# Optimization experiments

Hardware: AMD Instinct MI355X
Metric: run time of the kernel (lower is better)

## Reference

```python
import jax, jax.numpy as jnp
import numpy as np
import math

NH, KS, KR, VS, HID, RS = 8, 32, 8, 32, 256, 16
TOTAL = 2 * KS + VS + KR  # 104


def setup_inputs() -> dict:
    key = jax.random.key(0)
    ks = jax.random.split(key, 10)
    B, S = 4, 512
    H = jax.random.normal(ks[0], (B, S, HID), dtype=jnp.float32)
    route_data = jax.random.normal(ks[1], (B, S, S, RS), dtype=jnp.float32)
    attention_mask = jnp.zeros((B, 1, 1, S), dtype=jnp.float32)
    W_qkv = jax.random.normal(ks[2], (NH * TOTAL, HID), dtype=jnp.float32) * 0.02
    Wd = jax.random.normal(ks[3], (NH * KR, RS), dtype=jnp.float32) * 0.02
    Wroute = jax.random.normal(ks[4], (NH * VS, RS), dtype=jnp.float32) * 0.02
    W_out = jax.random.normal(ks[5], (HID, NH * VS), dtype=jnp.float32) * 0.02
    b_out = jnp.zeros((HID,), dtype=jnp.float32)
    ln_w = jnp.ones((HID,), dtype=jnp.float32)
    ln_b = jnp.zeros((HID,), dtype=jnp.float32)
    return {"H": H, "route_data": route_data, "attention_mask": attention_mask,
            "W_qkv": W_qkv, "Wd": Wd, "Wroute": Wroute,
            "W_out": W_out, "b_out": b_out, "ln_w": ln_w, "ln_b": ln_b}


def reference(H, route_data, attention_mask, W_qkv, Wd, Wroute, W_out, b_out, ln_w, ln_b):
    B, S, _ = H.shape
    # fused QKVQr projection: [B,S,NH,TOTAL] -> [B,NH,S,TOTAL]
    H2 = (H @ W_qkv.T).reshape(B, S, NH, TOTAL).transpose(0, 2, 1, 3)
    Qn = H2[..., :KS]
    Kn = H2[..., KS:2 * KS]
    V = H2[..., 2 * KS:2 * KS + VS]
    Qr = H2[..., 2 * KS + VS:]
    # route keys: [B,i,j,NH,KR]
    Kr = (route_data @ Wd.T).reshape(B, S, S, NH, KR)
    QKr = jnp.einsum('bhik,bijhk->bhij', Qr, Kr)
    scale = 1.0 / math.sqrt(KS + KR)
    scores = scale * (jnp.einsum('bhik,bhjk->bhij', Qn, Kn) + QKr) + attention_mask
    probs = jax.nn.softmax(scores, axis=-1)
    ctx = jnp.einsum('bhij,bhjv->bhiv', probs, V)
    # route values: [B,i,j,NH,VS]
    Vr = (route_data @ Wroute.T).reshape(B, S, S, NH, VS)
    ctx = ctx + jnp.einsum('bhij,bijhv->bhiv', probs, Vr)
    ctx = ctx.transpose(0, 2, 1, 3).reshape(B, S, NH * VS)
    # output projection + TF-style LayerNorm, residual added AFTER norm
    out = ctx @ W_out.T + b_out
    u = out.mean(-1, keepdims=True)
    s = ((out - u) ** 2).mean(-1, keepdims=True)
    ln = ln_w * (out - u) / jnp.sqrt(s + 1e-12) + ln_b
    return ln + H
```

## Files before the change

kernel.cpp:

```cpp
#include <hip/hip_runtime.h>
#include <cmath>

#define B_    4
#define S_    512
#define NH_   8
#define TOT_  104
#define NQKV_ 832
#define ROWS_ 2048

typedef float f32x4 __attribute__((ext_vector_type(4)));
typedef short short8 __attribute__((ext_vector_type(8)));

__device__ inline float bfu2f(unsigned int bits16) {
  union { unsigned int i; float f; } v; v.i = bits16 << 16; return v.f;
}
__device__ inline unsigned short f2bf(float f) {
  union { float f; unsigned int i; } v; v.f = f;
  unsigned int r = v.i + 0x7fffu + ((v.i >> 16) & 1u);
  return (unsigned short)(r >> 16);
}
__device__ inline short8 ld8(const unsigned short* p) {
  union { uint4 u; short8 s; } v; v.u = *(const uint4*)p; return v.s;
}
__device__ inline short8 pk8(float4 a, float4 b) {
  union { unsigned short us[8]; short8 s; } v;
  v.us[0]=f2bf(a.x); v.us[1]=f2bf(a.y); v.us[2]=f2bf(a.z); v.us[3]=f2bf(a.w);
  v.us[4]=f2bf(b.x); v.us[5]=f2bf(b.y); v.us[6]=f2bf(b.z); v.us[7]=f2bf(b.w);
  return v.s;
}

__global__ __launch_bounds__(256) void k1_qkv(const float* __restrict__ Hin,
                                              const float* __restrict__ Wqkv,
                                              unsigned short* __restrict__ Qnb,
                                              unsigned short* __restrict__ Knb,
                                              unsigned short* __restrict__ Vtb,
                                              float* __restrict__ Qr) {
  const int t = threadIdx.x;
  const int w = t >> 6, l = t & 63;
  const int lm = l & 15, lk = (l >> 4) << 3;
  const int i0 = blockIdx.y * 64 + w * 16;
  const int n0 = blockIdx.x * 64;
  f32x4 acc[4] = {};
  for (int k0 = 0; k0 < 256; k0 += 32) {
    const float* ap = Hin + (size_t)(i0 + lm) * 256 + k0 + lk;
    short8 a = pk8(*(const float4*)ap, *(const float4*)(ap + 4));
#pragma unroll
    for (int nf = 0; nf < 4; ++nf) {
      const float* bp = Wqkv + (size_t)(n0 + nf * 16 + lm) * 256 + k0 + lk;
      short8 b = pk8(*(const float4*)bp, *(const float4*)(bp + 4));
      acc[nf] = __builtin_amdgcn_mfma_f32_16x16x32_bf16(a, b, acc[nf], 0, 0, 0);
    }
  }
  const int rbase = i0 + ((l >> 4) << 2);
#pragma unroll
  for (int nf = 0; nf < 4; ++nf) {
#pragma unroll
    for (int r = 0; r < 4; ++r) {
      int row = rbase + r;
      int c = n0 + nf * 16 + lm;
      int b_ = row >> 9, i = row & 511;
      int h = c / 104, o = c - h * 104;
      float v = acc[nf][r];
      size_t bh = (size_t)(b_ * 8 + h);
      if (o < 32)       Qnb[(bh * 512 + i) * 32 + o] = f2bf(v);
      else if (o < 64)  Knb[(bh * 512 + i) * 32 + (o - 32)] = f2bf(v);
      else if (o < 96)  Vtb[(bh * 32 + (o - 64)) * 512 + i] = f2bf(v);
      else              Qr[(size_t)row * 64 + h * 8 + (o - 96)] = v;
    }
  }
}

__global__ __launch_bounds__(256) void k1c_qrr(const float* __restrict__ Qr,
                                               const float* __restrict__ Wd,
                                               float* __restrict__ qrrg) {
  int t = threadIdx.x;
  int row = blockIdx.x * 2 + (t >> 7);
  int c = t & 127, h = c >> 4, r = c & 15;
  float s = 0.f;
#pragma unroll
  for (int k = 0; k < 8; ++k)
    s += Qr[(size_t)row * 64 + h * 8 + k] * Wd[(h * 8 + k) * 16 + r];
  qrrg[(size_t)row * 128 + c] = s;
}

__global__ __launch_bounds__(256) void k2_qk(const unsigned short* __restrict__ Qnb,
                                             const unsigned short* __restrict__ Knb,
                                             unsigned short* __restrict__ sqk) {
  const int t = threadIdx.x;
  const int w = t >> 6, l = t & 63;
  const int lm = l & 15, lk = (l >> 4) << 3;
  const int bh = blockIdx.z;
  const int i0 = blockIdx.y * 64 + w * 16, j0 = blockIdx.x * 64;
  short8 a = ld8(Qnb + ((size_t)bh * 512 + i0 + lm) * 32 + lk);
  f32x4 acc[4] = {};
#pragma unroll
  for (int nf = 0; nf < 4; ++nf) {
    short8 b = ld8(Knb + ((size_t)bh * 512 + j0 + nf * 16 + lm) * 32 + lk);
    acc[nf] = __builtin_amdgcn_mfma_f32_16x16x32_bf16(a, b, acc[nf], 0, 0, 0);
  }
  const int rbase = i0 + ((l >> 4) << 2);
#pragma unroll
  for (int nf = 0; nf < 4; ++nf)
#pragma unroll
    for (int r = 0; r < 4; ++r)
      sqk[((size_t)bh * 512 + rbase + r) * 512 + j0 + nf * 16 + lm] = f2bf(acc[nf][r]);
}

__global__ __launch_bounds__(256) void k3_route(const float* __restrict__ rd,
                                                const unsigned short* __restrict__ sqk,
                                                const float* __restrict__ qrrg,
                                                const float* __restrict__ Wroute,
                                                const float* __restrict__ mask,
                                                unsigned short* __restrict__ probs,
                                                float* __restrict__ ctx) {
  __shared__ unsigned int rdp[512][10];
  __shared__ unsigned int sc_bf[8][257];
  __shared__ float qrr[8][16];
  __shared__ float prp[4][64][2];
  __shared__ float prf[8][16];
  const int t = threadIdx.x;
  const int row = blockIdx.x, b = row >> 9, i = row & 511;

  const float4* rp = (const float4*)(rd + (size_t)row * 8192);
#pragma unroll
  for (int q = 0; q < 8; ++q) {
    int idx = q * 256 + t;
    float4 v = rp[idx];
    int j = idx >> 2, u0 = (idx & 3) * 2;
    rdp[j][u0]     = (unsigned int)f2bf(v.x) | ((unsigned int)f2bf(v.y) << 16);
    rdp[j][u0 + 1] = (unsigned int)f2bf(v.z) | ((unsigned int)f2bf(v.w) << 16);
  }
  if (t < 128) ((float*)qrr)[t] = qrrg[(size_t)row * 128 + t];
  __syncthreads();

  const float scal = 0.15811388300841898f;
  {
    float rlo[16], rhi[16];
#pragma unroll
    for (int q = 0; q < 4; ++q) {
      uint2 ua = *(const uint2*)&rdp[t][q * 2];
      uint2 uc = *(const uint2*)&rdp[t + 256][q * 2];
      rlo[q*4]   = bfu2f(ua.x & 0xffffu); rlo[q*4+1] = bfu2f(ua.x >> 16);
      rlo[q*4+2] = bfu2f(ua.y & 0xffffu); rlo[q*4+3] = bfu2f(ua.y >> 16);
      rhi[q*4]   = bfu2f(uc.x & 0xffffu); rhi[q*4+1] = bfu2f(uc.x >> 16);
      rhi[q*4+2] = bfu2f(uc.y & 0xffffu); rhi[q*4+3] = bfu2f(uc.y >> 16);
    }
    float mlo = mask[b * 512 + t], mhi = mask[b * 512 + t + 256];
#pragma unroll
    for (int h = 0; h < 8; ++h) {
      float slo = 0.f, shi = 0.f;
#pragma unroll
      for (int r = 0; r < 16; ++r) { slo += qrr[h][r] * rlo[r]; shi += qrr[h][r] * rhi[r]; }
      const unsigned short* qp = sqk + ((size_t)(b * 8 + h) * 512 + i) * 512;
      float qlo = bfu2f(qp[t]), qhi = bfu2f(qp[t + 256]);
      float vlo = scal * (qlo + slo) + mlo;
      float vhi = scal * (qhi + shi) + mhi;
      sc_bf[h][t] = (unsigned int)f2bf(vlo) | ((unsigned int)f2bf(vhi) << 16);
    }
  }
  __syncthreads();

  const int wave = t >> 6, lane = t & 63;
  for (int hh = 0; hh < 2; ++hh) {
    int h = wave * 2 + hh;
    float vlo[4], vhi[4];
    float m = -1e30f;
#pragma unroll
    for (int cq = 0; cq < 4; ++cq) {
      unsigned int u = sc_bf[h][lane + 64 * cq];
      vlo[cq] = bfu2f(u & 0xffffu); vhi[cq] = bfu2f(u >> 16);
      m = fmaxf(m, fmaxf(vlo[cq], vhi[cq]));
    }
#pragma unroll
    for (int o = 32; o; o >>= 1) m = fmaxf(m, __shfl_xor(m, o));
    float ssum = 0.f;
#pragma unroll
    for (int cq = 0; cq < 4; ++cq) {
      vlo[cq] = __expf(vlo[cq] - m); vhi[cq] = __expf(vhi[cq] - m);
      ssum += vlo[cq] + vhi[cq];
    }
#pragma unroll
    for (int o = 32; o; o >>= 1) ssum += __shfl_xor(ssum, o);
    float inv = 1.0f / ssum;
    unsigned short* pout = probs + ((size_t)(b * 8 + h) * 512 + i) * 512;
#pragma unroll
    for (int cq = 0; cq < 4; ++cq) {
      int jj = lane + 64 * cq;
      unsigned short plo = f2bf(vlo[cq] * inv), phi = f2bf(vhi[cq] * inv);
      pout[jj] = plo; pout[jj + 256] = phi;
      sc_bf[h][jj] = (unsigned int)plo | ((unsigned int)phi << 16);
    }
  }
  __syncthreads();

  {
    int c = t & 63, qj = t >> 6;
    int h = c >> 3, ru = c & 7;
    float p0 = 0.f, p1 = 0.f;
    for (int jj = qj * 64; jj < qj * 64 + 64; ++jj) {
      unsigned int u = sc_bf[h][jj];
      unsigned int rr = rdp[jj][ru];
      unsigned int r2 = rdp[jj + 256][ru];
      float plo = bfu2f(u & 0xffffu), phi = bfu2f(u >> 16);
      p0 += plo * bfu2f(rr & 0xffffu) + phi * bfu2f(r2 & 0xffffu);
      p1 += plo * bfu2f(rr >> 16)     + phi * bfu2f(r2 >> 16);
    }
    prp[qj][c][0] = p0; prp[qj][c][1] = p1;
  }
  __syncthreads();
  if (t < 128) {
    int h = t >> 4, r = t & 15;
    int c = h * 8 + (r >> 1), part = r & 1;
    prf[h][r] = prp[0][c][part] + prp[1][c][part] + prp[2][c][part] + prp[3][c][part];
  }
  __syncthreads();

  {
    int h = t >> 5;
    float s = 0.f;
#pragma unroll
    for (int r = 0; r < 16; ++r) s += prf[h][r] * Wroute[t * 16 + r];
    ctx[(size_t)row * 256 + t] = s;
  }
}

__global__ __launch_bounds__(256) void k4_pv(const unsigned short* __restrict__ probs,
                                             const unsigned short* __restrict__ Vtb,
                                             float* __restrict__ ctx) {
  const int t = threadIdx.x;
  const int w = t >> 6, l = t & 63;
  const int lm = l & 15, lk = (l >> 4) << 3;
  const int bh = blockIdx.y;
  const int b = bh >> 3, h = bh & 7;
  const int irow = blockIdx.x * 64 + w * 16 + lm;
  const int kbase = blockIdx.z * 128;
  f32x4 acc[2] = {};
  for (int k0 = kbase; k0 < kbase + 128; k0 += 32) {
    short8 a = ld8(probs + ((size_t)bh * 512 + irow) * 512 + k0 + lk);
#pragma unroll
    for (int nf = 0; nf < 2; ++nf) {
      short8 bb = ld8(Vtb + ((size_t)bh * 32 + nf * 16 + lm) * 512 + k0 + lk);
      acc[nf] = __builtin_amdgcn_mfma_f32_16x16x32_bf16(a, bb, acc[nf], 0, 0, 0);
    }
  }
  const int rbase = blockIdx.x * 64 + w * 16 + ((l >> 4) << 2);
#pragma unroll
  for (int nf = 0; nf < 2; ++nf)
#pragma unroll
    for (int r = 0; r < 4; ++r) {
      size_t addr = ((size_t)b * 512 + rbase + r) * 256 + h * 32 + nf * 16 + lm;
      atomicAdd(&ctx[addr], acc[nf][r]);
    }
}

__global__ __launch_bounds__(256) void k5_out(const float* __restrict__ ctx,
                                              const float* __restrict__ Wout,
                                              const float* __restrict__ bout,
                                              const float* __restrict__ lnw,
                                              const float* __restrict__ lnb,
                                              const float* __restrict__ Hin,
                                              float* __restrict__ out) {
  __shared__ float buf[4][257];
  __shared__ float uarr[4], rarr[4];
  const int t = threadIdx.x;
  const int R0 = blockIdx.x * 4;
  {
    int sr = t >> 6, c0 = (t & 63) * 4;
    float4 a = *(const float4*)(ctx + (size_t)(R0 + sr) * 256 + c0);
    buf[sr][c0+0]=a.x; buf[sr][c0+1]=a.y; buf[sr][c0+2]=a.z; buf[sr][c0+3]=a.w;
  }
  __syncthreads();

  float o[4];
  {
    float bo = bout[t];
#pragma unroll
    for (int r = 0; r < 4; ++r) o[r] = bo;
  }
  const float4* wp = (const float4*)(Wout + (size_t)t * 256);
  for (int d4 = 0; d4 < 64; ++d4) {
    float4 w = wp[d4];
    int d = d4 * 4;
#pragma unroll
    for (int r = 0; r < 4; ++r)
      o[r] += buf[r][d]*w.x + buf[r][d+1]*w.y + buf[r][d+2]*w.z + buf[r][d+3]*w.w;
  }
  __syncthreads();
#pragma unroll
  for (int r = 0; r < 4; ++r) buf[r][t] = o[r];
  __syncthreads();
  {
    int wave = t >> 6, lane = t & 63;
    int r = wave;
    float s = 0.f, sq = 0.f;
#pragma unroll
    for (int c = 0; c < 4; ++c) {
      float x = buf[r][lane + 64*c];
      s += x; sq += x*x;
    }
#pragma unroll
    for (int off = 32; off; off >>= 1) {
      s += __shfl_xor(s, off);
      sq += __shfl_xor(sq, off);
    }
    if (lane == 0) {
      float u = s * (1.0f/256.0f);
      uarr[r] = u;
      rarr[r] = rsqrtf(sq * (1.0f/256.0f) - u*u + 1e-12f);
    }
  }
  __syncthreads();
  {
    float lw = lnw[t], lb = lnb[t];
#pragma unroll
    for (int r = 0; r < 4; ++r) {
      size_t R = R0 + r;
      out[R * 256 + t] = lw * (o[r] - uarr[r]) * rarr[r] + lb + Hin[R * 256 + t];
    }
  }
}

extern "C" void kernel_launch(void* const* d_in, const int* in_sizes, int n_in,
                              void* d_out, int out_size, void* d_ws, size_t ws_size,
                              hipStream_t stream) {
  const float* Hin    = (const float*)d_in[0];
  const float* rd     = (const float*)d_in[1];
  const float* mask   = (const float*)d_in[2];
  const float* Wqkv   = (const float*)d_in[3];
  const float* Wd     = (const float*)d_in[4];
  const float* Wroute = (const float*)d_in[5];
  const float* Wout   = (const float*)d_in[6];
  const float* bout   = (const float*)d_in[7];
  const float* lnw    = (const float*)d_in[8];
  const float* lnb    = (const float*)d_in[9];
  float* out = (float*)d_out;

  unsigned short* Qnb   = (unsigned short*)d_ws;
  unsigned short* Knb   = Qnb + 524288;
  unsigned short* Vtb   = Knb + 524288;
  unsigned short* sqk   = Vtb + 524288;
  unsigned short* probs = sqk + 8388608;
  float* Qr   = (float*)(probs + 8388608);
  float* qrrg = Qr + 131072;
  float* ctx  = qrrg + 262144;

  k1_qkv  <<<dim3(13, 32),      256, 0, stream>>>(Hin, Wqkv, Qnb, Knb, Vtb, Qr);
  k1c_qrr <<<1024,              256, 0, stream>>>(Qr, Wd, qrrg);
  k2_qk   <<<dim3(8, 8, 32),    256, 0, stream>>>(Qnb, Knb, sqk);
  k3_route<<<2048,              256, 0, stream>>>(rd, sqk, qrrg, Wroute, mask, probs, ctx);
  k4_pv   <<<dim3(8, 32, 4),    256, 0, stream>>>(probs, Vtb, ctx);
  k5_out  <<<512,               256, 0, stream>>>(ctx, Wout, bout, lnw, lnb, Hin, out);
}
```

Baseline: 196.8 us.

## Fold Wroute into output projection and drop atomics in PV kernel

Precomputes a combined weight Wco = Wout·Wroute per head so the route-value contribution is applied in the output kernel from the 128-wide prob-weighted route sums, instead of expanding them to 256 channels in the route kernel. The PV kernel now accumulates the full 512-long reduction per block and writes ctx directly, removing atomicAdd and the ctx zero-init dependency. The route kernel also loads route data into registers and computes scores from fp32 values rather than rereading bf16 from LDS, and prefetches QK scores early. This adds a small extra kernel and slightly more work in the output kernel, and changes rounding order.

```diff
diff --git a/kernel.cpp b/kernel.cpp
--- a/kernel.cpp
+++ b/kernel.cpp
@@ -19,6 +19,9 @@
   unsigned int r = v.i + 0x7fffu + ((v.i >> 16) & 1u);
   return (unsigned short)(r >> 16);
 }
+__device__ inline unsigned int pk2(float a, float b) {
+  return (unsigned int)f2bf(a) | ((unsigned int)f2bf(b) << 16);
+}
 __device__ inline short8 ld8(const unsigned short* p) {
   union { uint4 u; short8 s; } v; v.u = *(const uint4*)p; return v.s;
 }
@@ -27,6 +30,19 @@
   v.us[0]=f2bf(a.x); v.us[1]=f2bf(a.y); v.us[2]=f2bf(a.z); v.us[3]=f2bf(a.w);
   v.us[4]=f2bf(b.x); v.us[5]=f2bf(b.y); v.us[6]=f2bf(b.z); v.us[7]=f2bf(b.w);
   return v.s;
+}
+
+__global__ __launch_bounds__(256) void k0_wco(const float* __restrict__ Wout,
+                                              const float* __restrict__ Wroute,
+                                              float* __restrict__ Wco) {
+  const int t = threadIdx.x;
+  const int d = blockIdx.x * 2 + (t >> 7);
+  const int c = t & 127, h = c >> 4, r = c & 15;
+  float s = 0.f;
+#pragma unroll
+  for (int v = 0; v < 32; ++v)
+    s += Wout[(size_t)d * 256 + h * 32 + v] * Wroute[(h * 32 + v) * 16 + r];
+  Wco[(size_t)d * 128 + c] = s;
 }
 
 __global__ __launch_bounds__(256) void k1_qkv(const float* __restrict__ Hin,
@@ -109,11 +125,10 @@
 __global__ __launch_bounds__(256) void k3_route(const float* __restrict__ rd,
                                                 const unsigned short* __restrict__ sqk,
                                                 const float* __restrict__ qrrg,
-                                                const float* __restrict__ Wroute,
                                                 const float* __restrict__ mask,
                                                 unsigned short* __restrict__ probs,
-                                                float* __restrict__ ctx) {
-  __shared__ unsigned int rdp[512][10];
+                                                float* __restrict__ pr) {
+  __shared__ unsigned int rdp[512][9];
   __shared__ unsigned int sc_bf[8][257];
   __shared__ float qrr[8][16];
   __shared__ float prp[4][64][2];
@@ -121,42 +136,53 @@
   const int t = threadIdx.x;
   const int row = blockIdx.x, b = row >> 9, i = row & 511;
 
-  const float4* rp = (const float4*)(rd + (size_t)row * 8192);
-#pragma unroll
-  for (int q = 0; q < 8; ++q) {
-    int idx = q * 256 + t;
-    float4 v = rp[idx];
-    int j = idx >> 2, u0 = (idx & 3) * 2;
-    rdp[j][u0]     = (unsigned int)f2bf(v.x) | ((unsigned int)f2bf(v.y) << 16);
-    rdp[j][u0 + 1] = (unsigned int)f2bf(v.z) | ((unsigned int)f2bf(v.w) << 16);
-  }
+  const float4* rbase = (const float4*)(rd + (size_t)row * 8192);
+  float4 lo0 = rbase[t * 4 + 0], lo1 = rbase[t * 4 + 1];
+  float4 lo2 = rbase[t * 4 + 2], lo3 = rbase[t * 4 + 3];
+  float4 hi0 = rbase[(t + 256) * 4 + 0], hi1 = rbase[(t + 256) * 4 + 1];
+  float4 hi2 = rbase[(t + 256) * 4 + 2], hi3 = rbase[(t + 256) * 4 + 3];
+  const unsigned short* qb = sqk + ((size_t)(b * 8) * 512 + i) * 512;
+  unsigned int qk_lo[8], qk_hi[8];
+#pragma unroll
+  for (int h = 0; h < 8; ++h) {
+    qk_lo[h] = qb[(size_t)h * 512 * 512 + t];
+    qk_hi[h] = qb[(size_t)h * 512 * 512 + t + 256];
+  }
+  float mlo = mask[b * 512 + t], mhi = mask[b * 512 + t + 256];
   if (t < 128) ((float*)qrr)[t] = qrrg[(size_t)row * 128 + t];
+
+  rdp[t][0] = pk2(lo0.x, lo0.y); rdp[t][1] = pk2(lo0.z, lo0.w);
+  rdp[t][2] = pk2(lo1.x, lo1.y); rdp[t][3] = pk2(lo1.z, lo1.w);
+  rdp[t][4] = pk2(lo2.x, lo2.y); rdp[t][5] = pk2(lo2.z, lo2.w);
+  rdp[t][6] = pk2(lo3.x, lo3.y); rdp[t][7] = pk2(lo3.z, lo3.w);
+  rdp[t + 256][0] = pk2(hi0.x, hi0.y); rdp[t + 256][1] = pk2(hi0.z, hi0.w);
+  rdp[t + 256][2] = pk2(hi1.x, hi1.y); rdp[t + 256][3] = pk2(hi1.z, hi1.w);
+  rdp[t + 256][4] = pk2(hi2.x, hi2.y); rdp[t + 256][5] = pk2(hi2.z, hi2.w);
+  rdp[t + 256][6] = pk2(hi3.x, hi3.y); rdp[t + 256][7] = pk2(hi3.z, hi3.w);
   __syncthreads();
 
   const float scal = 0.15811388300841898f;
-  {
-    float rlo[16], rhi[16];
-#pragma unroll
-    for (int q = 0; q < 4; ++q) {
-      uint2 ua = *(const uint2*)&rdp[t][q * 2];
-      uint2 uc = *(const uint2*)&rdp[t + 256][q * 2];
-      rlo[q*4]   = bfu2f(ua.x & 0xffffu); rlo[q*4+1] = bfu2f(ua.x >> 16);
-      rlo[q*4+2] = bfu2f(ua.y & 0xffffu); rlo[q*4+3] = bfu2f(ua.y >> 16);
-      rhi[q*4]   = bfu2f(uc.x & 0xffffu); rhi[q*4+1] = bfu2f(uc.x >> 16);
-      rhi[q*4+2] = bfu2f(uc.y & 0xffffu); rhi[q*4+3] = bfu2f(uc.y >> 16);
-    }
-    float mlo = mask[b * 512 + t], mhi = mask[b * 512 + t + 256];
-#pragma unroll
-    for (int h = 0; h < 8; ++h) {
-      float slo = 0.f, shi = 0.f;
-#pragma unroll
-      for (int r = 0; r < 16; ++r) { slo += qrr[h][r] * rlo[r]; shi += qrr[h][r] * rhi[r]; }
-      const unsigned short* qp = sqk + ((size_t)(b * 8 + h) * 512 + i) * 512;
-      float qlo = bfu2f(qp[t]), qhi = bfu2f(qp[t + 256]);
-      float vlo = scal * (qlo + slo) + mlo;
-      float vhi = scal * (qhi + shi) + mhi;
-      sc_bf[h][t] = (unsigned int)f2bf(vlo) | ((unsigned int)f2bf(vhi) << 16);
-    }
+#pragma unroll
+  for (int h = 0; h < 8; ++h) {
+    float slo = qrr[h][0]  * lo0.x + qrr[h][1]  * lo0.y
+              + qrr[h][2]  * lo0.z + qrr[h][3]  * lo0.w
+              + qrr[h][4]  * lo1.x + qrr[h][5]  * lo1.y
+              + qrr[h][6]  * lo1.z + qrr[h][7]  * lo1.w
+              + qrr[h][8]  * lo2.x + qrr[h][9]  * lo2.y
+              + qrr[h][10] * lo2.z + qrr[h][11] * lo2.w
+              + qrr[h][12] * lo3.x + qrr[h][13] * lo3.y
+              + qrr[h][14] * lo3.z + qrr[h][15] * lo3.w;
+    float shi = qrr[h][0]  * hi0.x + qrr[h][1]  * hi0.y
+              + qrr[h][2]  * hi0.z + qrr[h][3]  * hi0.w
+              + qrr[h][4]  * hi1.x + qrr[h][5]  * hi1.y
+              + qrr[h][6]  * hi1.z + qrr[h][7]  * hi1.w
+              + qrr[h][8]  * hi2.x + qrr[h][9]  * hi2.y
+              + qrr[h][10] * hi2.z + qrr[h][11] * hi2.w
+              + qrr[h][12] * hi3.x + qrr[h][13] * hi3.y
+              + qrr[h][14] * hi3.z + qrr[h][15] * hi3.w;
+    float vlo = scal * (bfu2f(qk_lo[h]) + slo) + mlo;
+    float vhi = scal * (bfu2f(qk_hi[h]) + shi) + mhi;
+    sc_bf[h][t] = pk2(vlo, vhi);
   }
   __syncthreads();
 
@@ -214,14 +240,7 @@
     prf[h][r] = prp[0][c][part] + prp[1][c][part] + prp[2][c][part] + prp[3][c][part];
   }
   __syncthreads();
-
-  {
-    int h = t >> 5;
-    float s = 0.f;
-#pragma unroll
-    for (int r = 0; r < 16; ++r) s += prf[h][r] * Wroute[t * 16 + r];
-    ctx[(size_t)row * 256 + t] = s;
-  }
+  if (t < 128) pr[(size_t)row * 128 + t] = prf[t >> 4][t & 15];
 }
 
 __global__ __launch_bounds__(256) void k4_pv(const unsigned short* __restrict__ probs,
@@ -232,28 +251,23 @@
   const int lm = l & 15, lk = (l >> 4) << 3;
   const int bh = blockIdx.y;
   const int b = bh >> 3, h = bh & 7;
-  const int irow = blockIdx.x * 64 + w * 16 + lm;
-  const int kbase = blockIdx.z * 128;
-  f32x4 acc[2] = {};
-  for (int k0 = kbase; k0 < kbase + 128; k0 += 32) {
-    short8 a = ld8(probs + ((size_t)bh * 512 + irow) * 512 + k0 + lk);
-#pragma unroll
-    for (int nf = 0; nf < 2; ++nf) {
-      short8 bb = ld8(Vtb + ((size_t)bh * 32 + nf * 16 + lm) * 512 + k0 + lk);
-      acc[nf] = __builtin_amdgcn_mfma_f32_16x16x32_bf16(a, bb, acc[nf], 0, 0, 0);
-    }
-  }
-  const int rbase = blockIdx.x * 64 + w * 16 + ((l >> 4) << 2);
-#pragma unroll
-  for (int nf = 0; nf < 2; ++nf)
-#pragma unroll
-    for (int r = 0; r < 4; ++r) {
-      size_t addr = ((size_t)b * 512 + rbase + r) * 256 + h * 32 + nf * 16 + lm;
-      atomicAdd(&ctx[addr], acc[nf][r]);
-    }
+  const int i0 = blockIdx.x * 32 + (w & 1) * 16;
+  const int v0 = (w >> 1) * 16;
+  f32x4 acc = {};
+  for (int k0 = 0; k0 < 512; k0 += 32) {
+    short8 a  = ld8(probs + ((size_t)bh * 512 + i0 + lm) * 512 + k0 + lk);
+    short8 bb = ld8(Vtb + ((size_t)bh * 32 + v0 + lm) * 512 + k0 + lk);
+    acc = __builtin_amdgcn_mfma_f32_16x16x32_bf16(a, bb, acc, 0, 0, 0);
+  }
+  const int rbase = i0 + ((l >> 4) << 2);
+#pragma unroll
+  for (int r = 0; r < 4; ++r)
+    ctx[((size_t)b * 512 + rbase + r) * 256 + h * 32 + v0 + lm] = acc[r];
 }
 
 __global__ __launch_bounds__(256) void k5_out(const float* __restrict__ ctx,
+                                              const float* __restrict__ pr,
+                                              const float* __restrict__ Wco,
                                               const float* __restrict__ Wout,
                                               const float* __restrict__ bout,
                                               const float* __restrict__ lnw,
@@ -261,6 +275,7 @@
                                               const float* __restrict__ Hin,
                                               float* __restrict__ out) {
   __shared__ float buf[4][257];
+  __shared__ float prb[4][128];
   __shared__ float uarr[4], rarr[4];
   const int t = threadIdx.x;
   const int R0 = blockIdx.x * 4;
@@ -268,6 +283,12 @@
     int sr = t >> 6, c0 = (t & 63) * 4;
     float4 a = *(const float4*)(ctx + (size_t)(R0 + sr) * 256 + c0);
     buf[sr][c0+0]=a.x; buf[sr][c0+1]=a.y; buf[sr][c0+2]=a.z; buf[sr][c0+3]=a.w;
+  }
+#pragma unroll
+  for (int k = 0; k < 2; ++k) {
+    int e = k * 256 + t;
+    int sr = e >> 7, c = e & 127;
+    prb[sr][c] = pr[(size_t)(R0 + sr) * 128 + c];
   }
   __syncthreads();
 
@@ -284,6 +305,14 @@
 #pragma unroll
     for (int r = 0; r < 4; ++r)
       o[r] += buf[r][d]*w.x + buf[r][d+1]*w.y + buf[r][d+2]*w.z + buf[r][d+3]*w.w;
+  }
+  const float4* wc = (const float4*)(Wco + (size_t)t * 128);
+  for (int c4 = 0; c4 < 32; ++c4) {
+    float4 w = wc[c4];
+    int c = c4 * 4;
+#pragma unroll
+    for (int r = 0; r < 4; ++r)
+      o[r] += prb[r][c]*w.x + prb[r][c+1]*w.y + prb[r][c+2]*w.z + prb[r][c+3]*w.w;
   }
   __syncthreads();
 #pragma unroll
@@ -343,11 +372,14 @@
   float* Qr   = (float*)(probs + 8388608);
   float* qrrg = Qr + 131072;
   float* ctx  = qrrg + 262144;
-
-  k1_qkv  <<<dim3(13, 32),      256, 0, stream>>>(Hin, Wqkv, Qnb, Knb, Vtb, Qr);
-  k1c_qrr <<<1024,              256, 0, stream>>>(Qr, Wd, qrrg);
-  k2_qk   <<<dim3(8, 8, 32),    256, 0, stream>>>(Qnb, Knb, sqk);
-  k3_route<<<2048,              256, 0, stream>>>(rd, sqk, qrrg, Wroute, mask, probs, ctx);
-  k4_pv   <<<dim3(8, 32, 4),    256, 0, stream>>>(probs, Vtb, ctx);
-  k5_out  <<<512,               256, 0, stream>>>(ctx, Wout, bout, lnw, lnb, Hin, out);
-}
+  float* prg  = ctx + 524288;
+  float* Wco  = prg + 262144;
+
+  k0_wco  <<<128,            256, 0, stream>>>(Wout, Wroute, Wco);
+  k1_qkv  <<<dim3(13, 32),   256, 0, stream>>>(Hin, Wqkv, Qnb, Knb, Vtb, Qr);
+  k1c_qrr <<<1024,           256, 0, stream>>>(Qr, Wd, qrrg);
+  k2_qk   <<<dim3(8, 8, 32), 256, 0, stream>>>(Qnb, Knb, sqk);
+  k3_route<<<2048,           256, 0, stream>>>(rd, sqk, qrrg, mask, probs, prg);
+  k4_pv   <<<dim3(16, 32),   256, 0, stream>>>(probs, Vtb, ctx);
+  k5_out  <<<512,            256, 0, stream>>>(ctx, prg, Wco, Wout, bout, lnw, lnb, Hin, out);
+}
```

Measured after the change: 196.1 us. Within noise of the previous version (-0.4%).
